# Optimization experiments

Measured on AMD Instinct MI355X. Metric: run time of the kernel, lower is better.

Reference implementation:

```python
import jax, jax.numpy as jnp
import numpy as np

B, S, DIM, LW, CHUNK = 4, 4096, 512, 512, 64


def _l2n(x):
    n = jnp.sqrt(jnp.sum(x * x, axis=-1, keepdims=True))
    return x / jnp.maximum(n, 1e-12)


def setup_inputs() -> dict:
    key = jax.random.key(0)
    k = jax.random.split(key, 10)
    s = 1.0 / np.sqrt(DIM)
    return {
        "x": jax.random.normal(k[0], (B, S, DIM), jnp.float32),
        "Wq": jax.random.normal(k[1], (DIM, DIM), jnp.float32) * s,
        "Wk": jax.random.normal(k[2], (DIM, DIM), jnp.float32) * s,
        "Wv": jax.random.normal(k[3], (DIM, DIM), jnp.float32) * s,
        "init_w1": jax.random.normal(k[4], (LW, DIM), jnp.float32) * 0.02,
        "init_b1": jnp.zeros((LW,), jnp.float32),
        "init_w2": jax.random.normal(k[5], (DIM, LW), jnp.float32) * 0.02,
        "init_b2": jnp.zeros((DIM,), jnp.float32),
        "alpha_w": jax.random.normal(k[6], (DIM,), jnp.float32) * s,
        "alpha_b": jnp.full((1,), -5.0, jnp.float32),
        "eta_w": jax.random.normal(k[7], (DIM,), jnp.float32) * s,
        "eta_b": jnp.full((1,), 2.0, jnp.float32),
        "theta_w": jax.random.normal(k[8], (DIM,), jnp.float32) * s,
        "theta_b": jnp.full((1,), -4.6, jnp.float32),
        "chunk_size": CHUNK,
    }


def reference(x, Wq, Wk, Wv, init_w1, init_b1, init_w2, init_b2,
              alpha_w, alpha_b, eta_w, eta_b, theta_w, theta_b, chunk_size):
    b, s, d = x.shape
    c = int(chunk_size)
    nC = s // c
    lw = init_w1.shape[0]
    # per-sample memory params (broadcast of shared init) + zero momentum
    w1 = jnp.broadcast_to(init_w1, (b, lw, d))
    b1 = jnp.broadcast_to(init_b1, (b, lw))
    w2 = jnp.broadcast_to(init_w2, (b, d, lw))
    b2 = jnp.broadcast_to(init_b2, (b, d))
    mom = (jnp.zeros_like(w1), jnp.zeros_like(b1), jnp.zeros_like(w2), jnp.zeros_like(b2))
    xc = x.reshape(b, nC, c, d).transpose(1, 0, 2, 3)  # [nC, B, C, D]

    def step(carry, x_c):
        (w1, b1, w2, b2), (mw1, mb1, mw2, mb2) = carry
        q = _l2n(x_c @ Wq.T)
        k_ = _l2n(x_c @ Wk.T)
        v = x_c @ Wv.T
        # gates per token -> chunk-averaged, [B]
        a = jax.nn.sigmoid(x_c @ alpha_w + alpha_b).mean(axis=1)
        e = jax.nn.sigmoid(x_c @ eta_w + eta_b).mean(axis=1)
        t = jax.nn.sigmoid(x_c @ theta_w + theta_b).mean(axis=1)
        # retrieval with stale (chunk-constant) memory params
        hq = jax.nn.silu(jnp.einsum('bcd,bhd->bch', q, w1) + b1[:, None, :])
        y = jnp.einsum('bch,bdh->bcd', hq, w2) + b2[:, None, :]
        # per-token grads of mse(mlp(k), v) (mean over feature dim), chunk-averaged.
        # Analytic grads == autodiff of the tiny MLP; avoids [B,C,LW,D] intermediates.
        pre = jnp.einsum('bcd,bhd->bch', k_, w1) + b1[:, None, :]
        sg = jax.nn.sigmoid(pre)
        hk = pre * sg  # silu
        vp = jnp.einsum('bch,bdh->bcd', hk, w2) + b2[:, None, :]
        dvp = 2.0 * (vp - v) / d  # dL/d vp for mse over feature dim
        g_b2 = dvp.mean(axis=1)
        g_w2 = jnp.einsum('bcd,bch->bdh', dvp, hk) / c
        dh = jnp.einsum('bcd,bdh->bch', dvp, w2) * (sg * (1.0 + pre * (1.0 - sg)))
        g_b1 = dh.mean(axis=1)
        g_w1 = jnp.einsum('bch,bcd->bhd', dh, k_) / c
        a3, e3, t3 = a[:, None, None], e[:, None, None], t[:, None, None]
        a2, e2, t2 = a[:, None], e[:, None], t[:, None]
        nmw1 = e3 * mw1 - t3 * g_w1
        nmb1 = e2 * mb1 - t2 * g_b1
        nmw2 = e3 * mw2 - t3 * g_w2
        nmb2 = e2 * mb2 - t2 * g_b2
        nw1 = (1.0 - a3) * w1 + nmw1
        nb1 = (1.0 - a2) * b1 + nmb1
        nw2 = (1.0 - a3) * w2 + nmw2
        nb2 = (1.0 - a2) * b2 + nmb2
        return ((nw1, nb1, nw2, nb2), (nmw1, nmb1, nmw2, nmb2)), y

    _, ys = jax.lax.scan(step, ((w1, b1, w2, b2), mom), xc)
    return ys.transpose(1, 0, 2, 3).reshape(b, s, d)
```

## Files before the change

kernel.cpp:

```cpp
#include <hip/hip_runtime.h>
#include <hip/hip_bf16.h>

#define BB 4
#define SS 4096
#define DD 512
#define LWW 512
#define CC 64
#define NCH 64

typedef unsigned short u16;
using fragAB = __attribute__((ext_vector_type(8))) short;
using fragC  = __attribute__((ext_vector_type(4))) float;
using u16x4  = __attribute__((ext_vector_type(4))) short;

__device__ __forceinline__ short f2bf(float f){
  unsigned u = __float_as_uint(f);
  u = (u + 0x7FFFu + ((u >> 16) & 1u)) >> 16;
  return (short)u;
}
__device__ __forceinline__ float bf2f(short s){
  return __uint_as_float(((unsigned)(u16)s) << 16);
}
__device__ __forceinline__ fragC zeroC(){ fragC z = {0.f,0.f,0.f,0.f}; return z; }

__device__ __forceinline__ fragAB frag_bf16g(const u16* __restrict__ base, int ld, int r0, int k0, int lane){
  return *(const fragAB*)(base + (size_t)(r0 + (lane & 15)) * ld + k0 + ((lane >> 4) << 3));
}
__device__ __forceinline__ fragAB frag_lds(const short* base, int ld, int r0, int k0, int lane){
  return *(const fragAB*)(base + (r0 + (lane & 15)) * ld + k0 + ((lane >> 4) << 3));
}
#define MFMA16(a,b,c) __builtin_amdgcn_mfma_f32_16x16x32_bf16(a,b,c,0,0,0)

__device__ __forceinline__ void ld_sys(fragAB& r, const u16* p){
  asm volatile("global_load_dwordx4 %0, %1, off sc0 sc1" : "=v"(r) : "v"(p) : "memory");
}
__device__ __forceinline__ void st_sys2(u16* p, short v){
  asm volatile("global_store_short %0, %1, off sc0 sc1" :: "v"(p), "v"((unsigned)(u16)v) : "memory");
}
__device__ __forceinline__ void st_sys8(u16* p, u16x4 v){
  asm volatile("global_store_dwordx2 %0, %1, off sc0 sc1" :: "v"(p), "v"(v) : "memory");
}
#define WAITVM(N) do { asm volatile("s_waitcnt vmcnt(" #N ")" ::: "memory"); \
                       __builtin_amdgcn_sched_barrier(0); } while (0)

__device__ __forceinline__ const u16* taddr(const u16* base, int c, int kq){
  return base + (((size_t)((kq >> 4)*64 + c)) << 4) + (kq & 15);
}
__device__ __forceinline__ u16* taddrw(u16* base, int c, int kq){
  return base + (((size_t)((kq >> 4)*64 + c)) << 4) + (kq & 15);
}

__device__ __forceinline__ void bar_sync(unsigned* slots, unsigned phase, int tl){
  asm volatile("s_waitcnt vmcnt(0)" ::: "memory");
  __builtin_amdgcn_sched_barrier(0);
  __syncthreads();
  if (threadIdx.x == 0)
    __hip_atomic_store(slots + (size_t)tl*32, phase, __ATOMIC_RELAXED, __HIP_MEMORY_SCOPE_AGENT);
  if (threadIdx.x < 64){
    bool mine = threadIdx.x < 32;
    unsigned* sp = slots + (size_t)(threadIdx.x & 31)*32;
    for (;;){
      unsigned v = mine ? __hip_atomic_load(sp, __ATOMIC_RELAXED, __HIP_MEMORY_SCOPE_AGENT) : phase;
      if (__all((int)(v >= phase))) break;
      __builtin_amdgcn_s_sleep(1);
    }
  }
  __syncthreads();
}

__global__ __launch_bounds__(256) void k_cvt(const float* __restrict__ x,
    const float* __restrict__ Wq, const float* __restrict__ Wk, const float* __restrict__ Wv,
    u16* __restrict__ xb, u16* __restrict__ Wc, unsigned* __restrict__ bar){
  size_t i = (size_t)blockIdx.x * 256 + threadIdx.x;
  if (blockIdx.x == 0){
    for (int z = threadIdx.x; z < 4096; z += 256) bar[z] = 0u;
  }
  const size_t NX4 = (size_t)BB*SS*DD/4;
  const size_t NW4 = (size_t)DD*DD/4;
  if (i < NX4){
    float4 v = ((const float4*)x)[i];
    u16x4 o = { f2bf(v.x), f2bf(v.y), f2bf(v.z), f2bf(v.w) };
    *(u16x4*)(xb + 4*i) = o;
  } else if (i < NX4 + 3*NW4){
    size_t j = i - NX4;
    const float* src = (j < NW4) ? Wq : (j < 2*NW4) ? Wk : Wv;
    size_t jj = j % NW4;
    float4 v = ((const float4*)src)[jj];
    u16x4 o = { f2bf(v.x), f2bf(v.y), f2bf(v.z), f2bf(v.w) };
    *(u16x4*)(Wc + 4*j) = o;
  }
}

__global__ __launch_bounds__(256) void k_proj(const u16* __restrict__ xb,
    const u16* __restrict__ Wc,
    u16* __restrict__ Qb, u16* __restrict__ Kb, float* __restrict__ V){
  int mt = blockIdx.x / 12, nt = blockIdx.x % 12;
  int lane = threadIdx.x & 63, wid = threadIdx.x >> 6;
  int m0 = mt * 64 + wid * 16;
  const u16* Bp = Wc + (size_t)nt * 128 * DD;
  fragC acc[8];
#pragma unroll
  for (int i = 0; i < 8; ++i) acc[i] = zeroC();
  for (int k0 = 0; k0 < DD; k0 += 32){
    fragAB a = frag_bf16g(xb, DD, m0, k0, lane);
#pragma unroll
    for (int nf = 0; nf < 8; ++nf)
      acc[nf] = MFMA16(a, frag_bf16g(Bp, DD, nf*16, k0, lane), acc[nf]);
  }
#pragma unroll
  for (int nf = 0; nf < 8; ++nf){
#pragma unroll
    for (int r = 0; r < 4; ++r){
      int m = m0 + ((lane >> 4) << 2) + r;
      int col = nt*128 + nf*16 + (lane & 15);
      float v = acc[nf][r];
      if (nt < 4)      Qb[(size_t)m*DD + col]        = (u16)f2bf(v);
      else if (nt < 8) Kb[(size_t)m*DD + col - 512]  = (u16)f2bf(v);
      else             V [(size_t)m*DD + col - 1024] = v;
    }
  }
}

__global__ __launch_bounds__(256) void k_norm(u16* __restrict__ Qb, u16* __restrict__ Kb){
  int idx = blockIdx.x * 4 + (threadIdx.x >> 6);
  int lane = threadIdx.x & 63;
  u16* p = (idx < BB*SS ? Qb + (size_t)idx * DD
                        : Kb + (size_t)(idx - BB*SS) * DD) + lane * 8;
  fragAB v = *(const fragAB*)p;
  float f[8]; float s = 0.f;
#pragma unroll
  for (int i = 0; i < 8; ++i){ f[i] = bf2f(v[i]); s += f[i]*f[i]; }
#pragma unroll
  for (int o = 32; o > 0; o >>= 1) s += __shfl_xor(s, o, 64);
  float inv = 1.f / fmaxf(sqrtf(s), 1e-12f);
  fragAB o8;
#pragma unroll
  for (int i = 0; i < 8; ++i) o8[i] = f2bf(f[i] * inv);
  *(fragAB*)p = o8;
}

__global__ __launch_bounds__(256) void k_trans(const u16* __restrict__ Kb, u16* __restrict__ KT){
  __shared__ short tile[64][68];
  int blk = blockIdx.x;
  int b = blk >> 9, rem = blk & 511;
  int st = rem >> 3, dt = rem & 7;
  int s0 = st*64, d0 = dt*64;
  int sr = threadIdx.x & 63, q = threadIdx.x >> 6;
  const u16* src = Kb + ((size_t)b*SS + s0 + sr)*DD + d0 + q*16;
  fragAB v0 = *(const fragAB*)src;
  fragAB v1 = *(const fragAB*)(src + 8);
#pragma unroll
  for (int i = 0; i < 8; ++i){ tile[sr][q*16+i] = v0[i]; tile[sr][q*16+8+i] = v1[i]; }
  __syncthreads();
  fragAB o0, o1;
#pragma unroll
  for (int i = 0; i < 8; ++i){ o0[i] = tile[q*16+i][sr]; o1[i] = tile[q*16+8+i][sr]; }
  u16* dst = KT + ((size_t)b*DD + d0 + sr)*SS + s0 + q*16;
  *(fragAB*)dst = o0;
  *(fragAB*)(dst + 8) = o1;
}

__global__ __launch_bounds__(256) void k_gates(const float* __restrict__ x,
    const float* __restrict__ aw, const float* __restrict__ ab,
    const float* __restrict__ ew, const float* __restrict__ eb,
    const float* __restrict__ tw, const float* __restrict__ tb,
    float* __restrict__ aet){
  __shared__ float part[64][4][3];
  __shared__ float rowsig[64][3];
  int b = blockIdx.x >> 6, t = blockIdx.x & 63;
  int tid = threadIdx.x;
  int r = tid >> 2, p = tid & 3;
  const float4* xp = (const float4*)(x + ((size_t)b*SS + (size_t)t*CC + r) * DD + p * 128);
  const float4* a4 = (const float4*)(aw + p*128);
  const float4* e4 = (const float4*)(ew + p*128);
  const float4* t4 = (const float4*)(tw + p*128);
  float s0 = 0.f, s1 = 0.f, s2 = 0.f;
  for (int i = 0; i < 32; ++i){
    float4 xv = xp[i], av = a4[i], ev = e4[i], tv = t4[i];
    s0 += xv.x*av.x + xv.y*av.y + xv.z*av.z + xv.w*av.w;
    s1 += xv.x*ev.x + xv.y*ev.y + xv.z*ev.z + xv.w*ev.w;
    s2 += xv.x*tv.x + xv.y*tv.y + xv.z*tv.z + xv.w*tv.w;
  }
  part[r][p][0] = s0; part[r][p][1] = s1; part[r][p][2] = s2;
  __syncthreads();
  if (tid < 64){
    float a_ = part[tid][0][0]+part[tid][1][0]+part[tid][2][0]+part[tid][3][0] + ab[0];
    float e_ = part[tid][0][1]+part[tid][1][1]+part[tid][2][1]+part[tid][3][1] + eb[0];
    float t_ = part[tid][0][2]+part[tid][1][2]+part[tid][2][2]+part[tid][3][2] + tb[0];
    rowsig[tid][0] = 1.f/(1.f+expf(-a_));
    rowsig[tid][1] = 1.f/(1.f+expf(-e_));
    rowsig[tid][2] = 1.f/(1.f+expf(-t_));
  }
  __syncthreads();
  if (tid < 3){
    float s = 0.f;
    for (int i = 0; i < 64; ++i) s += rowsig[i][tid];
    aet[((size_t)b*NCH + t)*3 + tid] = s * (1.f/64.f);
  }
}

__global__ __launch_bounds__(512, 2) void k_scan(
    const u16* __restrict__ Qb, const u16* __restrict__ Kb, const u16* __restrict__ KTg,
    const float* __restrict__ V, const float* __restrict__ aet,
    const float* __restrict__ iw1, const float* __restrict__ ib1,
    const float* __restrict__ iw2, const float* __restrict__ ib2,
    u16* __restrict__ hkb, u16* __restrict__ hqs, u16* __restrict__ hkT,
    u16* __restrict__ dvpb, u16* __restrict__ w2Tb,
    float* __restrict__ out, unsigned* __restrict__ barb)
{
  __shared__ __align__(16) short s_w1[16*520];
  __shared__ __align__(16) short s_w2[16*520];
  __shared__ __align__(16) short s_pf[16*520];
  __shared__ __align__(16) short s_t[16*72];
  __shared__ float s_b1[16], s_mb1[16], s_b2[16], s_mb2[16];

  const int tid  = threadIdx.x;
  const int lane = tid & 63;
  const int wid  = tid >> 6;
  const int q    = lane >> 4;
  const int l15  = lane & 15;
  const int qk   = q << 3;
  const int b    = (blockIdx.x & 7) >> 1;
  const int tl   = ((blockIdx.x >> 3) << 1) | (blockIdx.x & 1);
  const int h0   = tl * 16;
  const int d0   = tl * 16;
  unsigned* slots = barb + (size_t)b * 1024;
  unsigned  ph   = 0;

  const u16* Kball = Kb  + (size_t)b*SS*DD;
  const u16* Qball = Qb  + (size_t)b*SS*DD;
  const u16* KTbat = KTg + (size_t)b*DD*SS;
  u16* hk_b  = hkb  + (size_t)b*CC*LWW;
  u16* hq_b  = hqs  + (size_t)b*CC*LWW;
  u16* hkT_b = hkT  + (size_t)b*LWW*CC;
  u16* dv_b  = dvpb + (size_t)b*CC*DD;
  const size_t W2TBUF = (size_t)BB*DD*LWW;

  float w1f[16], mw1f[16], w2f[16], mw2f[16], actr[4];

  {
    u16* w2T0 = w2Tb + (size_t)b*DD*LWW;
#pragma unroll
    for (int nf = 0; nf < 4; ++nf){
      u16x4 pk;
#pragma unroll
      for (int r = 0; r < 4; ++r){
        int hr = q*4 + r;
        int dcol = wid*64 + nf*16 + l15;
        float a = iw1[(size_t)(h0 + hr)*DD + dcol];
        w1f[nf*4+r] = a; mw1f[nf*4+r] = 0.f;
        s_w1[hr*520 + dcol] = f2bf(a);
        float c = iw2[(size_t)(d0 + hr)*LWW + dcol];
        w2f[nf*4+r] = c; mw2f[nf*4+r] = 0.f;
        s_w2[hr*520 + dcol] = f2bf(c);
        pk[r] = f2bf(c);
      }
      st_sys8(w2T0 + (size_t)(wid*64 + nf*16 + l15)*DD + d0 + q*4, pk);
    }
    if (tid < 16){
      s_b1[tid] = ib1[h0 + tid]; s_mb1[tid] = 0.f;
      s_b2[tid] = ib2[d0 + tid]; s_mb2[tid] = 0.f;
    }
#pragma unroll
    for (int r = 0; r < 4; ++r) actr[r] = 0.f;
    WAITVM(0);
    __syncthreads();
  }

  for (int t = 0; t < NCH; ++t){
    if (t > 0){
      fragAB kfr[8];
      {
        const u16* KTm = KTbat + (size_t)(t-1)*CC;
#pragma unroll
        for (int nf = 0; nf < 4; ++nf)
#pragma unroll
          for (int kk = 0; kk < 2; ++kk)
            kfr[nf*2+kk] = frag_bf16g(KTm, SS, wid*64 + nf*16, kk*32, lane);
      }
      if (wid < 4){
        fragAB fa[8];
        fragC a0 = zeroC();
#pragma unroll
        for (int j = 0; j < 8; ++j) ld_sys(fa[j], taddr(dv_b, wid*16 + l15, j*32 + qk));
        WAITVM(4);
#pragma unroll
        for (int j = 0; j < 4; ++j) a0 = MFMA16(fa[j], frag_lds(s_pf, 520, 0, j*32, lane), a0);
#pragma unroll
        for (int j = 0; j < 4; ++j) ld_sys(fa[j], taddr(dv_b, wid*16 + l15, (8+j)*32 + qk));
        WAITVM(4);
#pragma unroll
        for (int j = 0; j < 4; ++j) a0 = MFMA16(fa[4+j], frag_lds(s_pf, 520, 0, 128 + j*32, lane), a0);
#pragma unroll
        for (int j = 0; j < 4; ++j) ld_sys(fa[4+j], taddr(dv_b, wid*16 + l15, (12+j)*32 + qk));
        WAITVM(4);
#pragma unroll
        for (int j = 0; j < 4; ++j) a0 = MFMA16(fa[j], frag_lds(s_pf, 520, 0, 256 + j*32, lane), a0);
        WAITVM(0);
#pragma unroll
        for (int j = 0; j < 4; ++j) a0 = MFMA16(fa[4+j], frag_lds(s_pf, 520, 0, 384 + j*32, lane), a0);
#pragma unroll
        for (int r = 0; r < 4; ++r)
          s_t[l15*72 + wid*16 + q*4 + r] = f2bf(a0[r] * actr[r]);
      }
      __syncthreads();
      WAITVM(0);
      {
        fragC ag[4];
#pragma unroll
        for (int i = 0; i < 4; ++i) ag[i] = zeroC();
#pragma unroll
        for (int kk = 0; kk < 2; ++kk){
          fragAB af = frag_lds(s_t, 72, 0, kk*32, lane);
#pragma unroll
          for (int nf = 0; nf < 4; ++nf)
            ag[nf] = MFMA16(af, kfr[nf*2+kk], ag[nf]);
        }
        const float* g3 = aet + ((size_t)b*NCH + (t-1)) * 3;
        float ga = g3[0], ge = g3[1], gth = g3[2];
#pragma unroll
        for (int nf = 0; nf < 4; ++nf)
#pragma unroll
          for (int r = 0; r < 4; ++r){
            float g  = ag[nf][r] * (1.f/64.f);
            float m_ = ge*mw1f[nf*4+r] - gth*g;
            float w_ = (1.f-ga)*w1f[nf*4+r] + m_;
            mw1f[nf*4+r] = m_; w1f[nf*4+r] = w_;
            s_w1[(q*4+r)*520 + wid*64 + nf*16 + l15] = f2bf(w_);
          }
        if (tid < 16){
          const fragAB* row = (const fragAB*)(s_t + tid*72);
          float s = 0.f;
#pragma unroll
          for (int j = 0; j < 8; ++j){
            fragAB v = row[j];
#pragma unroll
            for (int i = 0; i < 8; ++i) s += bf2f(v[i]);
          }
          float gb = s * (1.f/64.f);
          float m_ = ge*s_mb1[tid] - gth*gb;
          float bn = (1.f-ga)*s_b1[tid] + m_;
          s_mb1[tid] = m_; s_b1[tid] = bn;
        }
      }
    }
    __syncthreads();
    {
      const u16* Ac = (wid < 4 ? Kball : Qball) + (size_t)t*CC*DD;
      int m0 = (wid & 3) * 16;
      fragC acc = zeroC();
      for (int k0 = 0; k0 < DD; k0 += 32)
        acc = MFMA16(frag_bf16g(Ac, DD, m0, k0, lane),
                     frag_lds(s_w1, 520, 0, k0, lane), acc);
      float bb = s_b1[l15];
      if (wid < 4){
        u16x4 pk;
#pragma unroll
        for (int r = 0; r < 4; ++r){
          int c = m0 + q*4 + r;
          float pre = acc[r] + bb;
          float sg  = 1.f/(1.f+expf(-pre));
          float hkv = pre * sg;
          actr[r]   = sg * (1.f + pre * (1.f - sg));
          short hb  = f2bf(hkv);
          st_sys2(taddrw(hk_b, c, h0 + l15), hb);
          pk[r] = hb;
        }
        st_sys8(hkT_b + (size_t)(h0 + l15)*CC + m0 + q*4, pk);
      } else {
#pragma unroll
        for (int r = 0; r < 4; ++r){
          int c = m0 + q*4 + r;
          float hqv = acc[r] + bb;
          float s2  = 1.f/(1.f+expf(-hqv));
          st_sys2(taddrw(hq_b, c, h0 + l15), f2bf(hqv * s2));
        }
      }
    }
    ph++; bar_sync(slots, ph, tl);

    {
      const u16* Ah = (wid < 4) ? hq_b : hk_b;
      int m0 = (wid & 3) * 16;
      fragC acc = zeroC();
      fragAB va[4], vb[4], hfr[8];
      float vv[4];
      if (wid >= 4){
#pragma unroll
        for (int r = 0; r < 4; ++r)
          vv[r] = V[((size_t)b*SS + (size_t)t*CC + m0 + q*4 + r)*DD + d0 + l15];
      }
#pragma unroll
      for (int j = 0; j < 4; ++j) ld_sys(va[j], taddr(Ah, m0 + l15, j*32 + qk));
#pragma unroll
      for (int j = 0; j < 4; ++j) ld_sys(vb[j], taddr(Ah, m0 + l15, 128 + j*32 + qk));
      WAITVM(4);
#pragma unroll
      for (int j = 0; j < 4; ++j) acc = MFMA16(va[j], frag_lds(s_w2, 520, 0, j*32, lane), acc);
#pragma unroll
      for (int j = 0; j < 4; ++j) ld_sys(va[j], taddr(Ah, m0 + l15, 256 + j*32 + qk));
      WAITVM(4);
#pragma unroll
      for (int j = 0; j < 4; ++j) acc = MFMA16(vb[j], frag_lds(s_w2, 520, 0, 128 + j*32, lane), acc);
#pragma unroll
      for (int j = 0; j < 4; ++j) ld_sys(vb[j], taddr(Ah, m0 + l15, 384 + j*32 + qk));
      WAITVM(4);
#pragma unroll
      for (int j = 0; j < 4; ++j) acc = MFMA16(va[j], frag_lds(s_w2, 520, 0, 256 + j*32, lane), acc);
#pragma unroll
      for (int nf = 0; nf < 4; ++nf)
#pragma unroll
        for (int kk = 0; kk < 2; ++kk)
          ld_sys(hfr[nf*2+kk], hkT_b + (size_t)(wid*64 + nf*16 + l15)*CC + kk*32 + qk);
      WAITVM(8);
#pragma unroll
      for (int j = 0; j < 4; ++j) acc = MFMA16(vb[j], frag_lds(s_w2, 520, 0, 384 + j*32, lane), acc);

      float bb = s_b2[l15];
      if (wid < 4){
#pragma unroll
        for (int r = 0; r < 4; ++r){
          int c = m0 + q*4 + r;
          __builtin_nontemporal_store(acc[r] + bb,
            &out[((size_t)b*SS + (size_t)t*CC + c)*DD + d0 + l15]);
        }
      } else {
#pragma unroll
        for (int r = 0; r < 4; ++r){
          int c = m0 + q*4 + r;
          float dvv = (acc[r] + bb - vv[r]) * (2.f/512.f);
          short db_ = f2bf(dvv);
          st_sys2(taddrw(dv_b, c, d0 + l15), db_);
          s_t[l15*72 + c] = db_;
        }
      }
      __syncthreads();
      WAITVM(0);
      {
        fragC ag[4];
#pragma unroll
        for (int i = 0; i < 4; ++i) ag[i] = zeroC();
#pragma unroll
        for (int kk = 0; kk < 2; ++kk){
          fragAB af = frag_lds(s_t, 72, 0, kk*32, lane);
#pragma unroll
          for (int nf = 0; nf < 4; ++nf)
            ag[nf] = MFMA16(af, hfr[nf*2+kk], ag[nf]);
        }
        const float* g3 = aet + ((size_t)b*NCH + t) * 3;
        float ga = g3[0], ge = g3[1], gth = g3[2];
        u16* w2Tn = w2Tb + (size_t)((t+1)&1)*W2TBUF + (size_t)b*DD*LWW;
#pragma unroll
        for (int nf = 0; nf < 4; ++nf){
          u16x4 pk;
#pragma unroll
          for (int r = 0; r < 4; ++r){
            float g  = ag[nf][r] * (1.f/64.f);
            float m_ = ge*mw2f[nf*4+r] - gth*g;
            float w_ = (1.f-ga)*w2f[nf*4+r] + m_;
            mw2f[nf*4+r] = m_; w2f[nf*4+r] = w_;
            short wb = f2bf(w_);
            s_w2[(q*4+r)*520 + wid*64 + nf*16 + l15] = wb;
            pk[r] = wb;
          }
          st_sys8(w2Tn + (size_t)(wid*64 + nf*16 + l15)*DD + d0 + q*4, pk);
        }
        if (tid < 16){
          const fragAB* row = (const fragAB*)(s_t + tid*72);
          float s = 0.f;
#pragma unroll
          for (int j = 0; j < 8; ++j){
            fragAB v = row[j];
#pragma unroll
            for (int i = 0; i < 8; ++i) s += bf2f(v[i]);
          }
          float gb = s * (1.f/64.f);
          float m_ = ge*s_mb2[tid] - gth*gb;
          float bn = (1.f-ga)*s_b2[tid] + m_;
          s_mb2[tid] = m_; s_b2[tid] = bn;
        }
        if (t + 1 < NCH){
          const u16* w2Tp = w2Tb + (size_t)(t&1)*W2TBUF + (size_t)b*DD*LWW;
          int hr = tid >> 5;
          int c0 = (tid & 31) << 4;
          const u16* src = w2Tp + (size_t)(h0 + hr)*DD + c0;
          fragAB t0, t1;
          ld_sys(t0, src);
          ld_sys(t1, src + 8);
          WAITVM(0);
          *(fragAB*)(s_pf + hr*520 + c0)     = t0;
          *(fragAB*)(s_pf + hr*520 + c0 + 8) = t1;
        }
      }
    }
    ph++; bar_sync(slots, ph, tl);
  }
}

extern "C" void kernel_launch(void* const* d_in, const int* in_sizes, int n_in,
                              void* d_out, int out_size, void* d_ws, size_t ws_size,
                              hipStream_t stream){
  const float* x   = (const float*)d_in[0];
  const float* Wq  = (const float*)d_in[1];
  const float* Wk  = (const float*)d_in[2];
  const float* Wv  = (const float*)d_in[3];
  const float* iw1 = (const float*)d_in[4];
  const float* ib1 = (const float*)d_in[5];
  const float* iw2 = (const float*)d_in[6];
  const float* ib2 = (const float*)d_in[7];
  const float* aw  = (const float*)d_in[8];
  const float* ab  = (const float*)d_in[9];
  const float* ew  = (const float*)d_in[10];
  const float* eb  = (const float*)d_in[11];
  const float* tw  = (const float*)d_in[12];
  const float* tb  = (const float*)d_in[13];
  float* out = (float*)d_out;

  float* fw = (float*)d_ws;
  float* V    = fw;  fw += (size_t)BB*SS*DD;
  float* aet  = fw;  fw += (size_t)BB*NCH*3 + 64;
  unsigned* bar = (unsigned*)fw; fw += 4096;
  u16* xb   = (u16*)fw;
  u16* Wc   = xb   + (size_t)BB*SS*DD;
  u16* Qb   = Wc   + (size_t)3*DD*DD;
  u16* Kb   = Qb   + (size_t)BB*SS*DD;
  u16* hkb  = Kb   + (size_t)BB*SS*DD;
  u16* hqs  = hkb  + (size_t)BB*CC*LWW;
  u16* hkT  = hqs  + (size_t)BB*CC*LWW;
  u16* dvpb = hkT  + (size_t)BB*LWW*CC;
  u16* w2Tb = dvpb + (size_t)BB*CC*DD;
  u16* KTg  = xb;

  k_cvt  <<<8960, 256, 0, stream>>>(x, Wq, Wk, Wv, xb, Wc, bar);
  k_proj <<<3072, 256, 0, stream>>>(xb, Wc, Qb, Kb, V);
  k_norm <<<8192, 256, 0, stream>>>(Qb, Kb);
  k_trans<<<2048, 256, 0, stream>>>(Kb, KTg);
  k_gates<<<256,  256, 0, stream>>>(x, aw, ab, ew, eb, tw, tb, aet);
  k_scan <<<128,  512, 0, stream>>>(Qb, Kb, KTg, V, aet, iw1, ib1, iw2, ib2,
                                    hkb, hqs, hkT, dvpb, w2Tb, out, bar);
}
```

Before: 1.597 ms.

## Stage hk/hq/dv tiles in LDS for coalesced stores; split dv·w2 across all waves

Per-element 2-byte system-coherent global stores of hk, hq and dvp are replaced by writes into LDS tiles. Those tiles are then flushed as contiguous 16-byte stores, relying on the tiled layout making each block's slice contiguous. The dh reduction previously done by four waves is split over all eight waves along K, with partial sums combined through shared memory. The w2T prefetch load is issued earlier so it overlaps the gradient MFMAs. This trades extra LDS traffic and barriers for fewer, wider global transactions and better wave utilization on the latency-critical scan path.

After: 1.438 ms. 10.0% less time.

```diff
diff --git a/kernel.cpp b/kernel.cpp
--- a/kernel.cpp
+++ b/kernel.cpp
@@ -34,19 +34,16 @@
 __device__ __forceinline__ void ld_sys(fragAB& r, const u16* p){
   asm volatile("global_load_dwordx4 %0, %1, off sc0 sc1" : "=v"(r) : "v"(p) : "memory");
 }
-__device__ __forceinline__ void st_sys2(u16* p, short v){
-  asm volatile("global_store_short %0, %1, off sc0 sc1" :: "v"(p), "v"((unsigned)(u16)v) : "memory");
-}
 __device__ __forceinline__ void st_sys8(u16* p, u16x4 v){
   asm volatile("global_store_dwordx2 %0, %1, off sc0 sc1" :: "v"(p), "v"(v) : "memory");
 }
+__device__ __forceinline__ void st_sys16(u16* p, fragAB v){
+  asm volatile("global_store_dwordx4 %0, %1, off sc0 sc1" :: "v"(p), "v"(v) : "memory");
+}
 #define WAITVM(N) do { asm volatile("s_waitcnt vmcnt(" #N ")" ::: "memory"); \
                        __builtin_amdgcn_sched_barrier(0); } while (0)
 
 __device__ __forceinline__ const u16* taddr(const u16* base, int c, int kq){
-  return base + (((size_t)((kq >> 4)*64 + c)) << 4) + (kq & 15);
-}
-__device__ __forceinline__ u16* taddrw(u16* base, int c, int kq){
   return base + (((size_t)((kq >> 4)*64 + c)) << 4) + (kq & 15);
 }
 
@@ -212,6 +209,9 @@
   __shared__ __align__(16) short s_w2[16*520];
   __shared__ __align__(16) short s_pf[16*520];
   __shared__ __align__(16) short s_t[16*72];
+  __shared__ __align__(16) short s_hk[64*16];
+  __shared__ __align__(16) short s_hq[64*16];
+  __shared__ float s_part[64][17];
   __shared__ float s_b1[16], s_mb1[16], s_b2[16], s_mb2[16];
 
   const int tid  = threadIdx.x;
@@ -278,33 +278,33 @@
           for (int kk = 0; kk < 2; ++kk)
             kfr[nf*2+kk] = frag_bf16g(KTm, SS, wid*64 + nf*16, kk*32, lane);
       }
-      if (wid < 4){
+      {
+        const int cst = (wid & 3) * 16;
+        const int kh  = (wid >> 2) * 256;
         fragAB fa[8];
         fragC a0 = zeroC();
 #pragma unroll
-        for (int j = 0; j < 8; ++j) ld_sys(fa[j], taddr(dv_b, wid*16 + l15, j*32 + qk));
+        for (int j = 0; j < 8; ++j) ld_sys(fa[j], taddr(dv_b, cst + l15, kh + j*32 + qk));
         WAITVM(4);
 #pragma unroll
-        for (int j = 0; j < 4; ++j) a0 = MFMA16(fa[j], frag_lds(s_pf, 520, 0, j*32, lane), a0);
-#pragma unroll
-        for (int j = 0; j < 4; ++j) ld_sys(fa[j], taddr(dv_b, wid*16 + l15, (8+j)*32 + qk));
-        WAITVM(4);
-#pragma unroll
-        for (int j = 0; j < 4; ++j) a0 = MFMA16(fa[4+j], frag_lds(s_pf, 520, 0, 128 + j*32, lane), a0);
-#pragma unroll
-        for (int j = 0; j < 4; ++j) ld_sys(fa[4+j], taddr(dv_b, wid*16 + l15, (12+j)*32 + qk));
-        WAITVM(4);
-#pragma unroll
-        for (int j = 0; j < 4; ++j) a0 = MFMA16(fa[j], frag_lds(s_pf, 520, 0, 256 + j*32, lane), a0);
+        for (int j = 0; j < 4; ++j) a0 = MFMA16(fa[j], frag_lds(s_pf, 520, 0, kh + j*32, lane), a0);
         WAITVM(0);
 #pragma unroll
-        for (int j = 0; j < 4; ++j) a0 = MFMA16(fa[4+j], frag_lds(s_pf, 520, 0, 384 + j*32, lane), a0);
-#pragma unroll
-        for (int r = 0; r < 4; ++r)
-          s_t[l15*72 + wid*16 + q*4 + r] = f2bf(a0[r] * actr[r]);
+        for (int j = 4; j < 8; ++j) a0 = MFMA16(fa[j], frag_lds(s_pf, 520, 0, kh + j*32, lane), a0);
+        if (wid >= 4){
+#pragma unroll
+          for (int r = 0; r < 4; ++r) s_part[cst + q*4 + r][l15] = a0[r];
+        }
+        __syncthreads();
+        if (wid < 4){
+#pragma unroll
+          for (int r = 0; r < 4; ++r){
+            float v = (a0[r] + s_part[cst + q*4 + r][l15]) * actr[r];
+            s_t[l15*72 + cst + q*4 + r] = f2bf(v);
+          }
+        }
       }
       __syncthreads();
-      WAITVM(0);
       {
         fragC ag[4];
 #pragma unroll
@@ -363,7 +363,7 @@
           float hkv = pre * sg;
           actr[r]   = sg * (1.f + pre * (1.f - sg));
           short hb  = f2bf(hkv);
-          st_sys2(taddrw(hk_b, c, h0 + l15), hb);
+          s_hk[c*16 + l15] = hb;
           pk[r] = hb;
         }
         st_sys8(hkT_b + (size_t)(h0 + l15)*CC + m0 + q*4, pk);
@@ -373,9 +373,16 @@
           int c = m0 + q*4 + r;
           float hqv = acc[r] + bb;
           float s2  = 1.f/(1.f+expf(-hqv));
-          st_sys2(taddrw(hq_b, c, h0 + l15), f2bf(hqv * s2));
-        }
-      }
+          s_hq[c*16 + l15] = f2bf(hqv * s2);
+        }
+      }
+    }
+    __syncthreads();
+    if (tid < 128){
+      st_sys16(hk_b + (size_t)tl*1024 + tid*8, *(const fragAB*)(s_hk + tid*8));
+    } else if (tid < 256){
+      int i = tid - 128;
+      st_sys16(hq_b + (size_t)tl*1024 + i*8, *(const fragAB*)(s_hq + i*8));
     }
     ph++; bar_sync(slots, ph, tl);
 
@@ -430,12 +437,14 @@
           int c = m0 + q*4 + r;
           float dvv = (acc[r] + bb - vv[r]) * (2.f/512.f);
           short db_ = f2bf(dvv);
-          st_sys2(taddrw(dv_b, c, d0 + l15), db_);
-          s_t[l15*72 + c] = db_;
+          s_hk[c*16 + l15] = db_;
+          s_t[l15*72 + c]  = db_;
         }
       }
       __syncthreads();
-      WAITVM(0);
+      if (wid < 4) { WAITVM(4); } else { WAITVM(0); }
+      if (tid < 128)
+        st_sys16(dv_b + (size_t)tl*1024 + tid*8, *(const fragAB*)(s_hk + tid*8));
       {
         fragC ag[4];
 #pragma unroll
@@ -446,6 +455,15 @@
 #pragma unroll
           for (int nf = 0; nf < 4; ++nf)
             ag[nf] = MFMA16(af, hfr[nf*2+kk], ag[nf]);
+        }
+        fragAB t0, t1;
+        int hr = tid >> 5;
+        int c0 = (tid & 31) << 4;
+        if (t + 1 < NCH){
+          const u16* w2Tp = w2Tb + (size_t)(t&1)*W2TBUF + (size_t)b*DD*LWW;
+          const u16* src = w2Tp + (size_t)(h0 + hr)*DD + c0;
+          ld_sys(t0, src);
+          ld_sys(t1, src + 8);
         }
         const float* g3 = aet + ((size_t)b*NCH + t) * 3;
         float ga = g3[0], ge = g3[1], gth = g3[2];
@@ -480,13 +498,6 @@
           s_mb2[tid] = m_; s_b2[tid] = bn;
         }
         if (t + 1 < NCH){
-          const u16* w2Tp = w2Tb + (size_t)(t&1)*W2TBUF + (size_t)b*DD*LWW;
-          int hr = tid >> 5;
-          int c0 = (tid & 31) << 4;
-          const u16* src = w2Tp + (size_t)(h0 + hr)*DD + c0;
-          fragAB t0, t1;
-          ld_sys(t0, src);
-          ld_sys(t1, src + 8);
           WAITVM(0);
           *(fragAB*)(s_pf + hr*520 + c0)     = t0;
           *(fragAB*)(s_pf + hr*520 + c0 + 8) = t1;
```
